# Performance work log

Hardware: AMD Instinct MI355X
Metric: run time of the kernel (lower is better)

The kernel has to match this reference:

```python
import jax, jax.numpy as jnp
import numpy as np

VOCAB, D, A, NEG = 32000, 200, 20, 2
NUM_USERS, NUM_ITEMS = 100000, 50000
R, L, B, NNZ = 4096, 128, 1024, 20480
EPS = 1e-12

def _norm(x, axis):
    n = jnp.sqrt(jnp.sum(x * x, axis=axis, keepdims=True))
    return x / jnp.maximum(n, EPS)

def setup_inputs() -> dict:
    key = jax.random.key(0)
    ks = jax.random.split(key, 20)
    rows_u = jax.random.randint(ks[5], (NNZ,), 0, B)
    cols_u = jax.random.randint(ks[6], (NNZ,), 0, R)
    rows_i = jax.random.randint(ks[7], (NNZ,), 0, B)
    cols_i = jax.random.randint(ks[8], (NNZ,), 0, R)
    return {
        "historical_review": jax.random.randint(ks[0], (R, L), 0, VOCAB),
        "neg_review": jax.random.randint(ks[1], (R * NEG, L), 0, VOCAB),
        "user": jax.random.randint(ks[2], (B,), 0, NUM_USERS),
        "item": jax.random.randint(ks[3], (B,), 0, NUM_ITEMS),
        "label": jax.random.uniform(ks[4], (B,), jnp.float32, 1.0, 5.0),
        "user_histor_index": jnp.stack([rows_u, cols_u]),
        "user_histor_value": jax.random.uniform(ks[9], (NNZ,), jnp.float32),
        "item_histor_index": jnp.stack([rows_i, cols_i]),
        "item_histor_value": jax.random.uniform(ks[10], (NNZ,), jnp.float32),
        "word_emb": jax.random.normal(ks[11], (VOCAB, D), jnp.float32),
        "Wm": jax.random.normal(ks[12], (D, D), jnp.float32) * 0.05,
        "Ww": jax.random.normal(ks[13], (A, D), jnp.float32) * 0.05,
        "bw": jnp.zeros((A,), jnp.float32),
        "Wt": jax.random.normal(ks[14], (D, A), jnp.float32) * 0.05,
        "fc_w": jax.random.uniform(ks[15], (1, 2 * D), jnp.float32, -0.05, 0.05),
        "fc_b": jnp.zeros((1,), jnp.float32),
        "fm_V": jax.random.uniform(ks[16], (2 * D, 10), jnp.float32, -0.05, 0.05),
        "b_users": jax.random.uniform(ks[17], (NUM_USERS, 1), jnp.float32, 0.0, 0.1),
        "b_items": jax.random.uniform(ks[18], (NUM_ITEMS, 1), jnp.float32, 0.0, 0.1),
    }

def reference(historical_review, neg_review, user, item, label,
              user_histor_index, user_histor_value,
              item_histor_index, item_histor_value,
              word_emb, Wm, Ww, bw, Wt, fc_w, fc_b, fm_V, b_users, b_items):
    # ABAE attention over each review
    e_w = word_emb[historical_review]              # (R, L, D)
    y_s = jnp.mean(e_w, axis=1)                    # (R, D)
    z_n = jnp.mean(word_emb[neg_review], axis=1)   # (R*NEG, D)
    dx = jnp.einsum('rld,rd->rl', e_w @ Wm.T, y_s) # (R, L)
    ax = jax.nn.softmax(dx, axis=1)
    # Faithful to source: view(R, D, L) is a raw reshape, not a transpose.
    z_s = jnp.einsum('rdl,rl->rd', e_w.reshape(R, D, L), ax)  # (R, D)
    p_t = z_s @ Ww.T + bw                          # (R, A)
    r_s = p_t @ Wt.T                               # (R, D)
    # cosine margin ranking loss
    c1 = jnp.sum(_norm(r_s, 1) * _norm(z_s, 1), axis=-1)      # (R,)
    c1 = jnp.repeat(c1, NEG)                                   # (R*NEG,)
    c2 = jnp.sum(_norm(z_n.reshape(R, NEG, D), 2) * _norm(r_s, 1)[:, None, :], axis=-1).reshape(-1)
    abae_out_loss = jax.nn.relu(c2 - c1 + 1.0)     # margin=1, target=+1
    J_loss = jnp.mean(abae_out_loss)
    # aspect-matrix orthogonality regularizer
    Tn = _norm(Wt, 0)                              # normalize columns (dim=0)
    U_loss = jnp.mean((Tn.T @ Tn - jnp.eye(A, dtype=Wt.dtype)) ** 2)
    # sparse (B, R) @ (R, D) aggregation via segment_sum
    user_aspect_embed = jax.ops.segment_sum(
        user_histor_value[:, None] * r_s[user_histor_index[1]],
        user_histor_index[0], num_segments=B)      # (B, D)
    item_aspect_embed = jax.ops.segment_sum(
        item_histor_value[:, None] * r_s[item_histor_index[1]],
        item_histor_index[0], num_segments=B)      # (B, D)
    input_vec = jnp.concatenate([user_aspect_embed, item_aspect_embed], axis=1)  # (B, 2D)
    fm_linear = input_vec @ fc_w.T + fc_b          # (B, 1)
    fm_i1 = (input_vec @ fm_V) ** 2
    fm_i2 = (input_vec ** 2) @ (fm_V ** 2)
    # NOTE: faithful to source, the quadratic term is summed over the whole batch (scalar)
    fm_output = 0.5 * jnp.sum(fm_i1 - fm_i2) + fm_linear + b_users[user] + b_items[item]
    prediction = fm_output.squeeze(1)              # (B,)
    rating_loss = (prediction - label) ** 2
    mse_loss = jnp.mean(rating_loss)
    obj_loss = mse_loss + 0.01 * J_loss + 0.01 * U_loss
    return (obj_loss, rating_loss, abae_out_loss, prediction, user_aspect_embed, item_aspect_embed)
```

## Files before the change

### kernel.cpp

```cpp
#include <hip/hip_runtime.h>
#include <hip/hip_fp16.h>
#include <math.h>

#define R_TOT 4096
#define L_LEN 128
#define D_DIM 200
#define A_DIM 20
#define NEGK  2
#define B_SZ  1024
#define NNZ_C 20480
#define RN_TOT (R_TOT*NEGK)
#define S_TOT (R_TOT + RN_TOT)
#define VOCAB_C 32000
#define EPS_ 1e-12f
#define SLOT_CAP 64
#define NBUCK_BLK 160

__device__ __forceinline__ float4 unpack4(const uint2 u) {
  union { unsigned v; __half2 h; } c0, c1;
  c0.v = u.x; c1.v = u.y;
  const float2 f0 = __half22float2(c0.h);
  const float2 f1 = __half22float2(c1.h);
  return make_float4(f0.x, f0.y, f1.x, f1.y);
}

__global__ __launch_bounds__(256) void k_cast(
    const float* __restrict__ emb, ushort* __restrict__ emb_h, int* __restrict__ cnt)
{
  if (blockIdx.x == 0) {
    for (int i = threadIdx.x; i < 2*B_SZ; i += 256) cnt[i] = 0;
  }
  const int idx = blockIdx.x*256 + threadIdx.x;
  if (idx < (VOCAB_C*D_DIM)/4) {
    const float4 v = reinterpret_cast<const float4*>(emb)[idx];
    ushort4 o;
    o.x = __half_as_ushort(__float2half(v.x));
    o.y = __half_as_ushort(__float2half(v.y));
    o.z = __half_as_ushort(__float2half(v.z));
    o.w = __half_as_ushort(__float2half(v.w));
    reinterpret_cast<ushort4*>(emb_h)[idx] = o;
  }
}

__global__ __launch_bounds__(256, 8) void k_means2(
    const int* __restrict__ hist, const int* __restrict__ neg,
    const ushort* __restrict__ emb_h,
    float* __restrict__ ys_all, float* __restrict__ zn_all,
    const int* __restrict__ uidx, const float* __restrict__ uval,
    const int* __restrict__ iidx, const float* __restrict__ ival,
    int* __restrict__ cnt, int* __restrict__ scol, float* __restrict__ sval)
{
  const int sb = blockIdx.x;
  const int tid = threadIdx.x;

  if (sb >= S_TOT) {
    const int g = (sb - S_TOT)*256 + tid;
    if (g < NNZ_C) {
      const int b = uidx[g];
      const int slot = atomicAdd(&cnt[b], 1);
      if (slot < SLOT_CAP) {
        scol[b*SLOT_CAP + slot] = uidx[NNZ_C + g];
        sval[b*SLOT_CAP + slot] = uval[g];
      }
    } else {
      const int g2 = g - NNZ_C;
      const int b = iidx[g2];
      const int slot = atomicAdd(&cnt[B_SZ + b], 1);
      if (slot < SLOT_CAP) {
        scol[(B_SZ + b)*SLOT_CAP + slot] = iidx[NNZ_C + g2];
        sval[(B_SZ + b)*SLOT_CAP + slot] = ival[g2];
      }
    }
    return;
  }

  __shared__ int widx[L_LEN];
  __shared__ __align__(16) float part[8][D_DIM];
  const bool is_pos = (sb < R_TOT);
  const int* src = is_pos ? (hist + (size_t)sb*L_LEN)
                          : (neg + (size_t)(sb - R_TOT)*L_LEN);
  if (tid < L_LEN) widx[tid] = src[tid];
  __syncthreads();

  const int c5 = tid & 31;
  const int j  = tid >> 5;
  float4 sA = {0.f,0.f,0.f,0.f}, sB = {0.f,0.f,0.f,0.f};
  if (c5 < 25) {
    const size_t coff = 8*c5;
    #pragma unroll
    for (int k0 = 0; k0 < 16; k0 += 4) {
      const uint4 q0 = *reinterpret_cast<const uint4*>(
          emb_h + (size_t)widx[j + 8*(k0+0)]*D_DIM + coff);
      const uint4 q1 = *reinterpret_cast<const uint4*>(
          emb_h + (size_t)widx[j + 8*(k0+1)]*D_DIM + coff);
      const uint4 q2 = *reinterpret_cast<const uint4*>(
          emb_h + (size_t)widx[j + 8*(k0+2)]*D_DIM + coff);
      const uint4 q3 = *reinterpret_cast<const uint4*>(
          emb_h + (size_t)widx[j + 8*(k0+3)]*D_DIM + coff);
      float4 e;
      e = unpack4(make_uint2(q0.x,q0.y)); sA.x+=e.x; sA.y+=e.y; sA.z+=e.z; sA.w+=e.w;
      e = unpack4(make_uint2(q0.z,q0.w)); sB.x+=e.x; sB.y+=e.y; sB.z+=e.z; sB.w+=e.w;
      e = unpack4(make_uint2(q1.x,q1.y)); sA.x+=e.x; sA.y+=e.y; sA.z+=e.z; sA.w+=e.w;
      e = unpack4(make_uint2(q1.z,q1.w)); sB.x+=e.x; sB.y+=e.y; sB.z+=e.z; sB.w+=e.w;
      e = unpack4(make_uint2(q2.x,q2.y)); sA.x+=e.x; sA.y+=e.y; sA.z+=e.z; sA.w+=e.w;
      e = unpack4(make_uint2(q2.z,q2.w)); sB.x+=e.x; sB.y+=e.y; sB.z+=e.z; sB.w+=e.w;
      e = unpack4(make_uint2(q3.x,q3.y)); sA.x+=e.x; sA.y+=e.y; sA.z+=e.z; sA.w+=e.w;
      e = unpack4(make_uint2(q3.z,q3.w)); sB.x+=e.x; sB.y+=e.y; sB.z+=e.z; sB.w+=e.w;
    }
    *reinterpret_cast<float4*>(&part[j][8*c5])     = sA;
    *reinterpret_cast<float4*>(&part[j][8*c5 + 4]) = sB;
  }
  __syncthreads();
  float* dst = is_pos ? (ys_all + (size_t)sb*D_DIM)
                      : (zn_all + (size_t)(sb - R_TOT)*D_DIM);
  if (tid < D_DIM) {
    float a = 0.f;
    #pragma unroll
    for (int j2 = 0; j2 < 8; ++j2) a += part[j2][tid];
    dst[tid] = a * (1.0f/128.0f);
  }
}

#define KB_RT 16
__global__ __launch_bounds__(256, 2) void k_matvec(
    const float* __restrict__ ys_all, const float* __restrict__ Wm,
    float* __restrict__ vv_all)
{
  __shared__ float ysl[KB_RT][D_DIM];
  const int r0 = blockIdx.x * KB_RT;
  const int tid = threadIdx.x;
  for (int i = tid; i < KB_RT*D_DIM; i += 256)
    ysl[i / D_DIM][i % D_DIM] = ys_all[(size_t)r0*D_DIM + i];
  __syncthreads();
  if (tid < D_DIM) {
    float acc[KB_RT];
    #pragma unroll
    for (int r = 0; r < KB_RT; ++r) acc[r] = 0.f;
    #pragma unroll 4
    for (int k = 0; k < D_DIM; ++k) {
      const float w = Wm[k*D_DIM + tid];
      #pragma unroll
      for (int r = 0; r < KB_RT; ++r) acc[r] += ysl[r][k] * w;
    }
    #pragma unroll
    for (int r = 0; r < KB_RT; ++r)
      vv_all[(size_t)(r0 + r)*D_DIM + tid] = acc[r];
  }
}

__global__ __launch_bounds__(512, 6) void k_attn(
    const int* __restrict__ hist, const ushort* __restrict__ emb_h,
    const float* __restrict__ vv_all,
    const float* __restrict__ Ww, const float* __restrict__ bw,
    const float* __restrict__ Wt, const float* __restrict__ zn_all,
    float* __restrict__ rs_out, float* __restrict__ abae)
{
  __shared__ __align__(16) ushort ew[L_LEN*D_DIM];
  __shared__ __align__(16) float ax[L_LEN];
  __shared__ __align__(16) float zs[D_DIM];
  __shared__ __align__(16) float ubuf[240];
  int*   widx  = reinterpret_cast<int*>(ubuf);
  float* ptile = ubuf;
  float* red   = ubuf + 160;

  const int r = blockIdx.x;
  const int tid = threadIdx.x, lane = tid & 63, wv = tid >> 6;

  if (tid < L_LEN) widx[tid] = hist[r*L_LEN + tid];
  __syncthreads();

  {
    const int c5 = tid & 31;
    const int j  = tid >> 5;
    float4 v8a = {0,0,0,0}, v8b = {0,0,0,0};
    if (c5 < 25) {
      v8a = *reinterpret_cast<const float4*>(vv_all + (size_t)r*D_DIM + 8*c5);
      v8b = *reinterpret_cast<const float4*>(vv_all + (size_t)r*D_DIM + 8*c5 + 4);
    }
    float p0=0.f,p1=0.f,p2=0.f,p3=0.f,p4=0.f,p5=0.f,p6=0.f,p7=0.f;
    if (c5 < 25) {
      const size_t coff = 8*c5;
      #pragma unroll
      for (int k = 0; k < 8; ++k) {
        const int l = j + 16*k;
        const uint4 q = *reinterpret_cast<const uint4*>(
            emb_h + (size_t)widx[l]*D_DIM + coff);
        *reinterpret_cast<uint4*>(ew + l*D_DIM + coff) = q;
        const float4 e0 = unpack4(make_uint2(q.x, q.y));
        const float4 e1 = unpack4(make_uint2(q.z, q.w));
        const float d = e0.x*v8a.x + e0.y*v8a.y + e0.z*v8a.z + e0.w*v8a.w
                      + e1.x*v8b.x + e1.y*v8b.y + e1.z*v8b.z + e1.w*v8b.w;
        if (k==0) p0=d; else if (k==1) p1=d; else if (k==2) p2=d; else if (k==3) p3=d;
        else if (k==4) p4=d; else if (k==5) p5=d; else if (k==6) p6=d; else p7=d;
      }
    }
    #pragma unroll
    for (int o = 16; o > 0; o >>= 1) {
      p0 += __shfl_xor(p0, o); p1 += __shfl_xor(p1, o);
      p2 += __shfl_xor(p2, o); p3 += __shfl_xor(p3, o);
      p4 += __shfl_xor(p4, o); p5 += __shfl_xor(p5, o);
      p6 += __shfl_xor(p6, o); p7 += __shfl_xor(p7, o);
    }
    if (c5 == 0) {
      ax[j]      = p0; ax[j + 16]  = p1; ax[j + 32]  = p2; ax[j + 48]  = p3;
      ax[j + 64] = p4; ax[j + 80]  = p5; ax[j + 96]  = p6; ax[j + 112] = p7;
    }
  }
  __syncthreads();

  if (tid < 64) {
    float m = fmaxf(ax[tid], ax[tid+64]);
    #pragma unroll
    for (int o = 32; o > 0; o >>= 1) m = fmaxf(m, __shfl_xor(m, o));
    if (tid == 0) red[0] = m;
  }
  __syncthreads();
  const float M = red[0];
  if (tid < L_LEN) ax[tid] = expf(ax[tid] - M);
  __syncthreads();
  if (tid < 64) {
    float s = ax[tid] + ax[tid+64];
    #pragma unroll
    for (int o = 32; o > 0; o >>= 1) s += __shfl_xor(s, o);
    if (tid == 0) red[1] = s;
  }
  __syncthreads();
  const float Sinv = 1.0f / red[1];
  if (tid < L_LEN) ax[tid] *= Sinv;
  __syncthreads();

  {
    const int lq = lane & 15;
    const int quad = lane >> 4;
    const float4 ax8a = *reinterpret_cast<const float4*>(ax + 8*lq);
    const float4 ax8b = *reinterpret_cast<const float4*>(ax + 8*lq + 4);
    for (int dq = wv; dq < 50; dq += 8) {
      const int d0 = 4*dq + quad;
      const int f0 = (d0 << 7) + 8*lq;
      const uint4 q = *reinterpret_cast<const uint4*>(ew + f0);
      const float4 e0 = unpack4(make_uint2(q.x, q.y));
      const float4 e1 = unpack4(make_uint2(q.z, q.w));
      float a = e0.x*ax8a.x + e0.y*ax8a.y + e0.z*ax8a.z + e0.w*ax8a.w
              + e1.x*ax8b.x + e1.y*ax8b.y + e1.z*ax8b.z + e1.w*ax8b.w;
      #pragma unroll
      for (int o = 8; o > 0; o >>= 1) a += __shfl_xor(a, o);
      if (lq == 0) zs[d0] = a;
    }
  }
  __syncthreads();

  if (tid < 160) {
    const int a = tid % 20, j = tid / 20;
    float s = 0.f;
    #pragma unroll
    for (int i = 0; i < 25; ++i) {
      const int d = j + 8*i;
      s += zs[d] * Ww[a*D_DIM + d];
    }
    ptile[tid] = s;
  }
  __syncthreads();
  if (tid < A_DIM) {
    float s = bw[tid];
    #pragma unroll
    for (int j = 0; j < 8; ++j) s += ptile[j*20 + tid];
    red[2 + tid] = s;
  }
  __syncthreads();

  float rsd = 0.f, zsd = 0.f, zn0 = 0.f, zn1 = 0.f;
  if (tid < D_DIM) {
    float acc = 0.f;
    #pragma unroll
    for (int a = 0; a < A_DIM; ++a) acc += red[2+a] * Wt[tid*A_DIM + a];
    rsd = acc; zsd = zs[tid];
    rs_out[(size_t)r*D_DIM + tid] = acc;
    zn0 = zn_all[(size_t)(2*r)*D_DIM + tid];
    zn1 = zn_all[(size_t)(2*r + 1)*D_DIM + tid];
  }
  float a0 = rsd*rsd, a1 = zsd*zsd, a2 = rsd*zsd;
  float b0 = zn0*zn0, b1 = zn0*rsd, b2 = zn1*zn1, b3 = zn1*rsd;
  #pragma unroll
  for (int o = 32; o > 0; o >>= 1) {
    a0 += __shfl_xor(a0, o); a1 += __shfl_xor(a1, o); a2 += __shfl_xor(a2, o);
    b0 += __shfl_xor(b0, o); b1 += __shfl_xor(b1, o);
    b2 += __shfl_xor(b2, o); b3 += __shfl_xor(b3, o);
  }
  if ((tid & 63) == 0) {
    red[22+wv] = a0; red[30+wv] = a1; red[38+wv] = a2;
    red[46+wv] = b0; red[54+wv] = b1; red[62+wv] = b2; red[70+wv] = b3;
  }
  __syncthreads();
  if (tid == 0) {
    float s0=0.f,s1=0.f,s2=0.f,t0=0.f,t1=0.f,t2=0.f,t3=0.f;
    #pragma unroll
    for (int i = 0; i < 8; ++i) {
      s0 += red[22+i]; s1 += red[30+i]; s2 += red[38+i];
      t0 += red[46+i]; t1 += red[54+i]; t2 += red[62+i]; t3 += red[70+i];
    }
    const float nr = fmaxf(sqrtf(s0), EPS_);
    const float nz = fmaxf(sqrtf(s1), EPS_);
    const float c1 = s2 / (nr * nz);
    const float c2a = t1 / (fmaxf(sqrtf(t0), EPS_) * nr);
    const float c2b = t3 / (fmaxf(sqrtf(t2), EPS_) * nr);
    abae[2*r]     = fmaxf(c2a - c1 + 1.0f, 0.0f);
    abae[2*r + 1] = fmaxf(c2b - c1 + 1.0f, 0.0f);
  }
}

__global__ __launch_bounds__(512) void k_aggfm(
    const int* __restrict__ cnt, const int* __restrict__ scol,
    const float* __restrict__ sval, const float* __restrict__ rs,
    const float* __restrict__ fcw, const float* __restrict__ V,
    float* __restrict__ uae, float* __restrict__ iae,
    float* __restrict__ linb, float* __restrict__ quadb)
{
  __shared__ __align__(16) float ivec[2*D_DIM];
  __shared__ float redw[8];
  __shared__ float qpart[10];
  const int b = blockIdx.x;
  const int tid = threadIdx.x, lane = tid & 63, wv = tid >> 6;

  if (tid < D_DIM) {
    int n = cnt[b]; n = n < SLOT_CAP ? n : SLOT_CAP;
    const int* cols = scol + (size_t)b*SLOT_CAP;
    const float* vals = sval + (size_t)b*SLOT_CAP;
    float acc = 0.f;
    for (int j = 0; j < n; ++j) acc += vals[j] * rs[(size_t)cols[j]*D_DIM + tid];
    ivec[tid] = acc;
    uae[(size_t)b*D_DIM + tid] = acc;
  } else if (tid >= 256 && tid < 256 + D_DIM) {
    const int t = tid - 256;
    int n = cnt[B_SZ + b]; n = n < SLOT_CAP ? n : SLOT_CAP;
    const int* cols = scol + (size_t)(B_SZ + b)*SLOT_CAP;
    const float* vals = sval + (size_t)(B_SZ + b)*SLOT_CAP;
    float acc = 0.f;
    for (int j = 0; j < n; ++j) acc += vals[j] * rs[(size_t)cols[j]*D_DIM + t];
    ivec[D_DIM + t] = acc;
    iae[(size_t)b*D_DIM + t] = acc;
  }
  __syncthreads();

  float lv = 0.f;
  if (tid < 2*D_DIM) lv = ivec[tid] * fcw[tid];
  #pragma unroll
  for (int o = 32; o > 0; o >>= 1) lv += __shfl_xor(lv, o);
  if (lane == 0) redw[wv] = lv;

  {
    const int k = wv;
    float s1 = 0.f, s2 = 0.f;
    for (int f = lane; f < 2*D_DIM; f += 64) {
      const float x = ivec[f];
      const float vk = V[f*10 + k];
      s1 += x*vk; s2 += x*x*vk*vk;
    }
    #pragma unroll
    for (int o = 32; o > 0; o >>= 1) { s1 += __shfl_xor(s1,o); s2 += __shfl_xor(s2,o); }
    if (lane == 0) qpart[k] = s1*s1 - s2;
  }
  if (wv < 2) {
    const int k = 8 + wv;
    float s1 = 0.f, s2 = 0.f;
    for (int f = lane; f < 2*D_DIM; f += 64) {
      const float x = ivec[f];
      const float vk = V[f*10 + k];
      s1 += x*vk; s2 += x*x*vk*vk;
    }
    #pragma unroll
    for (int o = 32; o > 0; o >>= 1) { s1 += __shfl_xor(s1,o); s2 += __shfl_xor(s2,o); }
    if (lane == 0) qpart[k] = s1*s1 - s2;
  }
  __syncthreads();
  if (tid == 0) {
    float lin = 0.f;
    #pragma unroll
    for (int i = 0; i < 8; ++i) lin += redw[i];
    float q = 0.f;
    #pragma unroll
    for (int i = 0; i < 10; ++i) q += qpart[i];
    linb[b] = lin; quadb[b] = q;
  }
}

__global__ __launch_bounds__(1024) void k_final2(
    const float* __restrict__ quadb, const float* __restrict__ linb,
    const float* __restrict__ fcb, const int* __restrict__ user,
    const int* __restrict__ item, const float* __restrict__ busers,
    const float* __restrict__ bitems, const float* __restrict__ label,
    const float* __restrict__ Wt, const float* __restrict__ abae,
    float* __restrict__ pred, float* __restrict__ rl, float* __restrict__ obj)
{
  __shared__ float sA[16], sB[16], sC[16];
  __shared__ float cninv[A_DIM];
  __shared__ float quad_s;
  const int tid = threadIdx.x;
  const int lane = tid & 63;
  const int wv = tid >> 6;

  float q = quadb[tid];
  #pragma unroll
  for (int o = 32; o > 0; o >>= 1) q += __shfl_xor(q, o);
  if (lane == 0) sA[wv] = q;

  if (tid < A_DIM) {
    float s = 0.f;
    for (int d = 0; d < D_DIM; ++d) { const float w = Wt[d*A_DIM + tid]; s += w*w; }
    cninv[tid] = 1.0f / fmaxf(sqrtf(s), EPS_);
  }
  __syncthreads();
  if (wv == 0) {
    float s = (lane < 16) ? sA[lane] : 0.f;
    #pragma unroll
    for (int o = 32; o > 0; o >>= 1) s += __shfl_xor(s, o);
    if (lane == 0) quad_s = s;
  }
  __syncthreads();

  const float p = 0.5f*quad_s + linb[tid] + fcb[0]
                + busers[user[tid]] + bitems[item[tid]];
  pred[tid] = p;
  const float dd = p - label[tid];
  const float myrl = dd*dd;
  rl[tid] = myrl;

  float u = 0.f;
  if (tid < 400) {
    const int a = tid / 20, c = tid % 20;
    float dot = 0.f;
    for (int d = 0; d < D_DIM; ++d) dot += Wt[d*A_DIM + a]*Wt[d*A_DIM + c];
    const float g = dot*cninv[a]*cninv[c] - (a==c ? 1.0f : 0.0f);
    u = g*g;
  }
  float js = 0.f;
  #pragma unroll
  for (int j = 0; j < 8; ++j) js += abae[tid + 1024*j];
  float ms = myrl;

  #pragma unroll
  for (int o = 32; o > 0; o >>= 1) {
    u += __shfl_xor(u,o); js += __shfl_xor(js,o); ms += __shfl_xor(ms,o);
  }
  if (lane == 0) { sA[wv] = u; sB[wv] = js; sC[wv] = ms; }
  __syncthreads();
  if (tid == 0) {
    float U = 0.f, J = 0.f, Ms = 0.f;
    for (int i = 0; i < 16; ++i) { U += sA[i]; J += sB[i]; Ms += sC[i]; }
    obj[0] = Ms/1024.0f + 0.01f*(J/8192.0f) + 0.01f*(U/400.0f);
  }
}

extern "C" void kernel_launch(void* const* d_in, const int* in_sizes, int n_in,
                              void* d_out, int out_size, void* d_ws, size_t ws_size,
                              hipStream_t stream) {
  const int*   hist   = (const int*)  d_in[0];
  const int*   neg    = (const int*)  d_in[1];
  const int*   user   = (const int*)  d_in[2];
  const int*   item   = (const int*)  d_in[3];
  const float* label  = (const float*)d_in[4];
  const int*   uidx   = (const int*)  d_in[5];
  const float* uval   = (const float*)d_in[6];
  const int*   iidx   = (const int*)  d_in[7];
  const float* ival   = (const float*)d_in[8];
  const float* emb    = (const float*)d_in[9];
  const float* Wm     = (const float*)d_in[10];
  const float* Ww     = (const float*)d_in[11];
  const float* bw     = (const float*)d_in[12];
  const float* Wt     = (const float*)d_in[13];
  const float* fcw    = (const float*)d_in[14];
  const float* fcb    = (const float*)d_in[15];
  const float* V      = (const float*)d_in[16];
  const float* busers = (const float*)d_in[17];
  const float* bitems = (const float*)d_in[18];

  float* out  = (float*)d_out;
  float* obj  = out;
  float* rl   = out + 1;
  float* abae = out + 1 + B_SZ;
  float* pred = out + 1 + B_SZ + RN_TOT;
  float* uae  = pred + B_SZ;
  float* iae  = uae + (size_t)B_SZ*D_DIM;

  float* ws     = (float*)d_ws;
  float* rs     = ws;
  float* ys_all = rs + (size_t)R_TOT*D_DIM;
  float* zn_all = ys_all + (size_t)R_TOT*D_DIM;
  float* vv_all = zn_all + (size_t)RN_TOT*D_DIM;
  float* linb   = vv_all + (size_t)R_TOT*D_DIM;
  float* quadb  = linb + B_SZ;
  float* sval   = quadb + B_SZ;
  int*   scol   = (int*)(sval + (size_t)2*B_SZ*SLOT_CAP);
  int*   cnt    = scol + (size_t)2*B_SZ*SLOT_CAP;
  ushort* emb_h = (ushort*)(cnt + 2*B_SZ);

  const int cast_blocks = (VOCAB_C*D_DIM/4 + 255)/256;

  k_cast  <<<cast_blocks, 256, 0, stream>>>(emb, emb_h, cnt);
  k_means2<<<S_TOT + NBUCK_BLK, 256, 0, stream>>>(hist, neg, emb_h,
                                                  ys_all, zn_all,
                                                  uidx, uval, iidx, ival,
                                                  cnt, scol, sval);
  k_matvec<<<R_TOT/KB_RT, 256, 0, stream>>>(ys_all, Wm, vv_all);
  k_attn  <<<R_TOT, 512, 0, stream>>>(hist, emb_h, vv_all, Ww, bw, Wt,
                                      zn_all, rs, abae);
  k_aggfm <<<B_SZ, 512, 0, stream>>>(cnt, scol, sval, rs, fcw, V,
                                     uae, iae, linb, quadb);
  k_final2<<<1, 1024, 0, stream>>>(quadb, linb, fcb, user, item, busers, bitems,
                                   label, Wt, abae, pred, rl, obj);
}
```

Before: 312.5 us.

## Process four reviews per attention block with register prefetch of next embeddings

The attention kernel now handles four reviews per block in a loop. While it computes the current review, it prefetches the next review's word indices, fp16 embedding rows, vv vector and zn values into registers. The goal is to hide gather latency behind the softmax and reduction stages and to cut block launch and index-staging overhead. In exchange the grid has a quarter as many blocks, register pressure rises from holding eight uint4 prefetches, and occupancy and parallelism across the GPU's compute units may drop.

```diff
diff --git a/kernel.cpp b/kernel.cpp
--- a/kernel.cpp
+++ b/kernel.cpp
@@ -15,6 +15,7 @@
 #define EPS_ 1e-12f
 #define SLOT_CAP 64
 #define NBUCK_BLK 160
+#define NREV 4
 
 __device__ __forceinline__ float4 unpack4(const uint2 u) {
   union { unsigned v; __half2 h; } c0, c1;
@@ -159,41 +160,80 @@
   __shared__ __align__(16) float ax[L_LEN];
   __shared__ __align__(16) float zs[D_DIM];
   __shared__ __align__(16) float ubuf[240];
-  int*   widx  = reinterpret_cast<int*>(ubuf);
   float* ptile = ubuf;
   float* red   = ubuf + 160;
 
-  const int r = blockIdx.x;
   const int tid = threadIdx.x, lane = tid & 63, wv = tid >> 6;
-
-  if (tid < L_LEN) widx[tid] = hist[r*L_LEN + tid];
-  __syncthreads();
-
-  {
-    const int c5 = tid & 31;
-    const int j  = tid >> 5;
-    float4 v8a = {0,0,0,0}, v8b = {0,0,0,0};
-    if (c5 < 25) {
-      v8a = *reinterpret_cast<const float4*>(vv_all + (size_t)r*D_DIM + 8*c5);
-      v8b = *reinterpret_cast<const float4*>(vv_all + (size_t)r*D_DIM + 8*c5 + 4);
-    }
+  const int c5 = tid & 31;
+  const int j  = tid >> 5;
+  const bool act = (c5 < 25);
+  const int coff = 8*c5;
+  const int r0 = blockIdx.x * NREV;
+
+  uint4 q0,q1,q2,q3,q4,q5,q6,q7;
+  q0=q1=q2=q3=q4=q5=q6=q7=make_uint4(0,0,0,0);
+  float4 v8a = {0,0,0,0}, v8b = {0,0,0,0};
+  if (act) {
+    const int base = r0*L_LEN + j;
+    const int w0 = hist[base],     w1 = hist[base+16], w2 = hist[base+32], w3 = hist[base+48];
+    const int w4 = hist[base+64],  w5 = hist[base+80], w6 = hist[base+96], w7 = hist[base+112];
+    q0 = *reinterpret_cast<const uint4*>(emb_h + (size_t)w0*D_DIM + coff);
+    q1 = *reinterpret_cast<const uint4*>(emb_h + (size_t)w1*D_DIM + coff);
+    q2 = *reinterpret_cast<const uint4*>(emb_h + (size_t)w2*D_DIM + coff);
+    q3 = *reinterpret_cast<const uint4*>(emb_h + (size_t)w3*D_DIM + coff);
+    q4 = *reinterpret_cast<const uint4*>(emb_h + (size_t)w4*D_DIM + coff);
+    q5 = *reinterpret_cast<const uint4*>(emb_h + (size_t)w5*D_DIM + coff);
+    q6 = *reinterpret_cast<const uint4*>(emb_h + (size_t)w6*D_DIM + coff);
+    q7 = *reinterpret_cast<const uint4*>(emb_h + (size_t)w7*D_DIM + coff);
+    v8a = *reinterpret_cast<const float4*>(vv_all + (size_t)r0*D_DIM + coff);
+    v8b = *reinterpret_cast<const float4*>(vv_all + (size_t)r0*D_DIM + coff + 4);
+  }
+
+  for (int i = 0; i < NREV; ++i) {
+    const int r = r0 + i;
+
+    int w0n=0,w1n=0,w2n=0,w3n=0,w4n=0,w5n=0,w6n=0,w7n=0;
+    if (act && i < NREV-1) {
+      const int nb = (r+1)*L_LEN + j;
+      w0n = hist[nb];     w1n = hist[nb+16]; w2n = hist[nb+32]; w3n = hist[nb+48];
+      w4n = hist[nb+64];  w5n = hist[nb+80]; w6n = hist[nb+96]; w7n = hist[nb+112];
+    }
+
+    __syncthreads();
+
     float p0=0.f,p1=0.f,p2=0.f,p3=0.f,p4=0.f,p5=0.f,p6=0.f,p7=0.f;
-    if (c5 < 25) {
-      const size_t coff = 8*c5;
-      #pragma unroll
-      for (int k = 0; k < 8; ++k) {
-        const int l = j + 16*k;
-        const uint4 q = *reinterpret_cast<const uint4*>(
-            emb_h + (size_t)widx[l]*D_DIM + coff);
-        *reinterpret_cast<uint4*>(ew + l*D_DIM + coff) = q;
-        const float4 e0 = unpack4(make_uint2(q.x, q.y));
-        const float4 e1 = unpack4(make_uint2(q.z, q.w));
-        const float d = e0.x*v8a.x + e0.y*v8a.y + e0.z*v8a.z + e0.w*v8a.w
-                      + e1.x*v8b.x + e1.y*v8b.y + e1.z*v8b.z + e1.w*v8b.w;
-        if (k==0) p0=d; else if (k==1) p1=d; else if (k==2) p2=d; else if (k==3) p3=d;
-        else if (k==4) p4=d; else if (k==5) p5=d; else if (k==6) p6=d; else p7=d;
+    if (act) {
+      #define STG(K, Q, P) { \
+        *reinterpret_cast<uint4*>(ew + (j + 16*(K))*D_DIM + coff) = Q; \
+        const float4 e0_ = unpack4(make_uint2(Q.x, Q.y)); \
+        const float4 e1_ = unpack4(make_uint2(Q.z, Q.w)); \
+        P = e0_.x*v8a.x + e0_.y*v8a.y + e0_.z*v8a.z + e0_.w*v8a.w \
+          + e1_.x*v8b.x + e1_.y*v8b.y + e1_.z*v8b.z + e1_.w*v8b.w; }
+      STG(0,q0,p0) STG(1,q1,p1) STG(2,q2,p2) STG(3,q3,p3)
+      STG(4,q4,p4) STG(5,q5,p5) STG(6,q6,p6) STG(7,q7,p7)
+      #undef STG
+      if (i < NREV-1) {
+        q0 = *reinterpret_cast<const uint4*>(emb_h + (size_t)w0n*D_DIM + coff);
+        q1 = *reinterpret_cast<const uint4*>(emb_h + (size_t)w1n*D_DIM + coff);
+        q2 = *reinterpret_cast<const uint4*>(emb_h + (size_t)w2n*D_DIM + coff);
+        q3 = *reinterpret_cast<const uint4*>(emb_h + (size_t)w3n*D_DIM + coff);
+        q4 = *reinterpret_cast<const uint4*>(emb_h + (size_t)w4n*D_DIM + coff);
+        q5 = *reinterpret_cast<const uint4*>(emb_h + (size_t)w5n*D_DIM + coff);
+        q6 = *reinterpret_cast<const uint4*>(emb_h + (size_t)w6n*D_DIM + coff);
+        q7 = *reinterpret_cast<const uint4*>(emb_h + (size_t)w7n*D_DIM + coff);
       }
     }
+    float4 v8an = {0,0,0,0}, v8bn = {0,0,0,0};
+    if (act && i < NREV-1) {
+      v8an = *reinterpret_cast<const float4*>(vv_all + (size_t)(r+1)*D_DIM + coff);
+      v8bn = *reinterpret_cast<const float4*>(vv_all + (size_t)(r+1)*D_DIM + coff + 4);
+    }
+    float zn0 = 0.f, zn1 = 0.f;
+    if (tid < D_DIM) {
+      zn0 = zn_all[(size_t)(2*r)*D_DIM + tid];
+      zn1 = zn_all[(size_t)(2*r + 1)*D_DIM + tid];
+    }
+
     #pragma unroll
     for (int o = 16; o > 0; o >>= 1) {
       p0 += __shfl_xor(p0, o); p1 += __shfl_xor(p1, o);
@@ -205,106 +245,106 @@
       ax[j]      = p0; ax[j + 16]  = p1; ax[j + 32]  = p2; ax[j + 48]  = p3;
       ax[j + 64] = p4; ax[j + 80]  = p5; ax[j + 96]  = p6; ax[j + 112] = p7;
     }
-  }
-  __syncthreads();
-
-  if (tid < 64) {
-    float m = fmaxf(ax[tid], ax[tid+64]);
-    #pragma unroll
-    for (int o = 32; o > 0; o >>= 1) m = fmaxf(m, __shfl_xor(m, o));
-    if (tid == 0) red[0] = m;
-  }
-  __syncthreads();
-  const float M = red[0];
-  if (tid < L_LEN) ax[tid] = expf(ax[tid] - M);
-  __syncthreads();
-  if (tid < 64) {
-    float s = ax[tid] + ax[tid+64];
-    #pragma unroll
-    for (int o = 32; o > 0; o >>= 1) s += __shfl_xor(s, o);
-    if (tid == 0) red[1] = s;
-  }
-  __syncthreads();
-  const float Sinv = 1.0f / red[1];
-  if (tid < L_LEN) ax[tid] *= Sinv;
-  __syncthreads();
-
-  {
-    const int lq = lane & 15;
-    const int quad = lane >> 4;
-    const float4 ax8a = *reinterpret_cast<const float4*>(ax + 8*lq);
-    const float4 ax8b = *reinterpret_cast<const float4*>(ax + 8*lq + 4);
-    for (int dq = wv; dq < 50; dq += 8) {
-      const int d0 = 4*dq + quad;
-      const int f0 = (d0 << 7) + 8*lq;
-      const uint4 q = *reinterpret_cast<const uint4*>(ew + f0);
-      const float4 e0 = unpack4(make_uint2(q.x, q.y));
-      const float4 e1 = unpack4(make_uint2(q.z, q.w));
-      float a = e0.x*ax8a.x + e0.y*ax8a.y + e0.z*ax8a.z + e0.w*ax8a.w
-              + e1.x*ax8b.x + e1.y*ax8b.y + e1.z*ax8b.z + e1.w*ax8b.w;
-      #pragma unroll
-      for (int o = 8; o > 0; o >>= 1) a += __shfl_xor(a, o);
-      if (lq == 0) zs[d0] = a;
-    }
-  }
-  __syncthreads();
-
-  if (tid < 160) {
-    const int a = tid % 20, j = tid / 20;
-    float s = 0.f;
-    #pragma unroll
-    for (int i = 0; i < 25; ++i) {
-      const int d = j + 8*i;
-      s += zs[d] * Ww[a*D_DIM + d];
-    }
-    ptile[tid] = s;
-  }
-  __syncthreads();
-  if (tid < A_DIM) {
-    float s = bw[tid];
-    #pragma unroll
-    for (int j = 0; j < 8; ++j) s += ptile[j*20 + tid];
-    red[2 + tid] = s;
-  }
-  __syncthreads();
-
-  float rsd = 0.f, zsd = 0.f, zn0 = 0.f, zn1 = 0.f;
-  if (tid < D_DIM) {
-    float acc = 0.f;
-    #pragma unroll
-    for (int a = 0; a < A_DIM; ++a) acc += red[2+a] * Wt[tid*A_DIM + a];
-    rsd = acc; zsd = zs[tid];
-    rs_out[(size_t)r*D_DIM + tid] = acc;
-    zn0 = zn_all[(size_t)(2*r)*D_DIM + tid];
-    zn1 = zn_all[(size_t)(2*r + 1)*D_DIM + tid];
-  }
-  float a0 = rsd*rsd, a1 = zsd*zsd, a2 = rsd*zsd;
-  float b0 = zn0*zn0, b1 = zn0*rsd, b2 = zn1*zn1, b3 = zn1*rsd;
-  #pragma unroll
-  for (int o = 32; o > 0; o >>= 1) {
-    a0 += __shfl_xor(a0, o); a1 += __shfl_xor(a1, o); a2 += __shfl_xor(a2, o);
-    b0 += __shfl_xor(b0, o); b1 += __shfl_xor(b1, o);
-    b2 += __shfl_xor(b2, o); b3 += __shfl_xor(b3, o);
-  }
-  if ((tid & 63) == 0) {
-    red[22+wv] = a0; red[30+wv] = a1; red[38+wv] = a2;
-    red[46+wv] = b0; red[54+wv] = b1; red[62+wv] = b2; red[70+wv] = b3;
-  }
-  __syncthreads();
-  if (tid == 0) {
-    float s0=0.f,s1=0.f,s2=0.f,t0=0.f,t1=0.f,t2=0.f,t3=0.f;
-    #pragma unroll
-    for (int i = 0; i < 8; ++i) {
-      s0 += red[22+i]; s1 += red[30+i]; s2 += red[38+i];
-      t0 += red[46+i]; t1 += red[54+i]; t2 += red[62+i]; t3 += red[70+i];
-    }
-    const float nr = fmaxf(sqrtf(s0), EPS_);
-    const float nz = fmaxf(sqrtf(s1), EPS_);
-    const float c1 = s2 / (nr * nz);
-    const float c2a = t1 / (fmaxf(sqrtf(t0), EPS_) * nr);
-    const float c2b = t3 / (fmaxf(sqrtf(t2), EPS_) * nr);
-    abae[2*r]     = fmaxf(c2a - c1 + 1.0f, 0.0f);
-    abae[2*r + 1] = fmaxf(c2b - c1 + 1.0f, 0.0f);
+    __syncthreads();
+
+    if (tid < 64) {
+      float m = fmaxf(ax[tid], ax[tid+64]);
+      #pragma unroll
+      for (int o = 32; o > 0; o >>= 1) m = fmaxf(m, __shfl_xor(m, o));
+      if (tid == 0) red[0] = m;
+    }
+    __syncthreads();
+    const float M = red[0];
+    if (tid < L_LEN) ax[tid] = expf(ax[tid] - M);
+    __syncthreads();
+    if (tid < 64) {
+      float s = ax[tid] + ax[tid+64];
+      #pragma unroll
+      for (int o = 32; o > 0; o >>= 1) s += __shfl_xor(s, o);
+      if (tid == 0) red[1] = s;
+    }
+    __syncthreads();
+    const float Sinv = 1.0f / red[1];
+    if (tid < L_LEN) ax[tid] *= Sinv;
+    __syncthreads();
+
+    {
+      const int lq = lane & 15;
+      const int quad = lane >> 4;
+      const float4 ax8a = *reinterpret_cast<const float4*>(ax + 8*lq);
+      const float4 ax8b = *reinterpret_cast<const float4*>(ax + 8*lq + 4);
+      for (int dq = wv; dq < 50; dq += 8) {
+        const int d0 = 4*dq + quad;
+        const int f0 = (d0 << 7) + 8*lq;
+        const uint4 q = *reinterpret_cast<const uint4*>(ew + f0);
+        const float4 e0 = unpack4(make_uint2(q.x, q.y));
+        const float4 e1 = unpack4(make_uint2(q.z, q.w));
+        float a = e0.x*ax8a.x + e0.y*ax8a.y + e0.z*ax8a.z + e0.w*ax8a.w
+                + e1.x*ax8b.x + e1.y*ax8b.y + e1.z*ax8b.z + e1.w*ax8b.w;
+        #pragma unroll
+        for (int o = 8; o > 0; o >>= 1) a += __shfl_xor(a, o);
+        if (lq == 0) zs[d0] = a;
+      }
+    }
+    __syncthreads();
+
+    if (tid < 160) {
+      const int a = tid % 20, jj = tid / 20;
+      float s = 0.f;
+      #pragma unroll
+      for (int ii = 0; ii < 25; ++ii) {
+        const int d = jj + 8*ii;
+        s += zs[d] * Ww[a*D_DIM + d];
+      }
+      ptile[tid] = s;
+    }
+    __syncthreads();
+    if (tid < A_DIM) {
+      float s = bw[tid];
+      #pragma unroll
+      for (int jj = 0; jj < 8; ++jj) s += ptile[jj*20 + tid];
+      red[2 + tid] = s;
+    }
+    __syncthreads();
+
+    float rsd = 0.f, zsd = 0.f;
+    if (tid < D_DIM) {
+      float acc = 0.f;
+      #pragma unroll
+      for (int a = 0; a < A_DIM; ++a) acc += red[2+a] * Wt[tid*A_DIM + a];
+      rsd = acc; zsd = zs[tid];
+      rs_out[(size_t)r*D_DIM + tid] = acc;
+    } else { zn0 = 0.f; zn1 = 0.f; }
+    float a0 = rsd*rsd, a1 = zsd*zsd, a2 = rsd*zsd;
+    float b0 = zn0*zn0, b1 = zn0*rsd, b2 = zn1*zn1, b3 = zn1*rsd;
+    #pragma unroll
+    for (int o = 32; o > 0; o >>= 1) {
+      a0 += __shfl_xor(a0, o); a1 += __shfl_xor(a1, o); a2 += __shfl_xor(a2, o);
+      b0 += __shfl_xor(b0, o); b1 += __shfl_xor(b1, o);
+      b2 += __shfl_xor(b2, o); b3 += __shfl_xor(b3, o);
+    }
+    if ((tid & 63) == 0) {
+      red[22+wv] = a0; red[30+wv] = a1; red[38+wv] = a2;
+      red[46+wv] = b0; red[54+wv] = b1; red[62+wv] = b2; red[70+wv] = b3;
+    }
+    __syncthreads();
+    if (tid == 0) {
+      float s0=0.f,s1=0.f,s2=0.f,t0=0.f,t1=0.f,t2=0.f,t3=0.f;
+      #pragma unroll
+      for (int ii = 0; ii < 8; ++ii) {
+        s0 += red[22+ii]; s1 += red[30+ii]; s2 += red[38+ii];
+        t0 += red[46+ii]; t1 += red[54+ii]; t2 += red[62+ii]; t3 += red[70+ii];
+      }
+      const float nr = fmaxf(sqrtf(s0), EPS_);
+      const float nz = fmaxf(sqrtf(s1), EPS_);
+      const float c1 = s2 / (nr * nz);
+      const float c2a = t1 / (fmaxf(sqrtf(t0), EPS_) * nr);
+      const float c2b = t3 / (fmaxf(sqrtf(t2), EPS_) * nr);
+      abae[2*r]     = fmaxf(c2a - c1 + 1.0f, 0.0f);
+      abae[2*r + 1] = fmaxf(c2b - c1 + 1.0f, 0.0f);
+    }
+
+    v8a = v8an; v8b = v8bn;
   }
 }
 
@@ -501,8 +541,8 @@
                                                   uidx, uval, iidx, ival,
                                                   cnt, scol, sval);
   k_matvec<<<R_TOT/KB_RT, 256, 0, stream>>>(ys_all, Wm, vv_all);
-  k_attn  <<<R_TOT, 512, 0, stream>>>(hist, emb_h, vv_all, Ww, bw, Wt,
-                                      zn_all, rs, abae);
+  k_attn  <<<R_TOT/NREV, 512, 0, stream>>>(hist, emb_h, vv_all, Ww, bw, Wt,
+                                           zn_all, rs, abae);
   k_aggfm <<<B_SZ, 512, 0, stream>>>(cnt, scol, sval, rs, fcw, V,
                                      uae, iae, linb, quadb);
   k_final2<<<1, 1024, 0, stream>>>(quadb, linb, fcb, user, item, busers, bitems,
```

After: 630.5 us. 2.02x slower.

## Batch gather loads and trim softmax barriers in means and attention kernels

Applied to the files above, without the earlier changes.

The mean kernel now issues eight independent embedding-row loads before accumulating, replacing the previous batches of four, to raise memory-level parallelism. The attention kernel hoists the vv and zn loads ahead of the first barrier and issues all eight row gathers up front. It fuses the softmax exp and sum into one pass, folding normalization into the zs write so two barriers disappear. The final reduction now uses shuffles instead of a serial loop on one thread. Occupancy hint for k_attn drops from 6 to 4 waves per SIMD to allow more registers. The cost is higher register pressure and possibly fewer resident blocks.

```diff
diff --git a/kernel.cpp b/kernel.cpp
--- a/kernel.cpp
+++ b/kernel.cpp
@@ -41,6 +41,12 @@
     reinterpret_cast<ushort4*>(emb_h)[idx] = o;
   }
 }
+
+#define ACC8(Q) { \
+  const float4 e0_ = unpack4(make_uint2((Q).x,(Q).y)); \
+  const float4 e1_ = unpack4(make_uint2((Q).z,(Q).w)); \
+  sA.x+=e0_.x; sA.y+=e0_.y; sA.z+=e0_.z; sA.w+=e0_.w; \
+  sB.x+=e1_.x; sB.y+=e1_.y; sB.z+=e1_.z; sB.w+=e1_.w; }
 
 __global__ __launch_bounds__(256, 8) void k_means2(
     const int* __restrict__ hist, const int* __restrict__ neg,
@@ -87,26 +93,24 @@
   float4 sA = {0.f,0.f,0.f,0.f}, sB = {0.f,0.f,0.f,0.f};
   if (c5 < 25) {
     const size_t coff = 8*c5;
-    #pragma unroll
-    for (int k0 = 0; k0 < 16; k0 += 4) {
-      const uint4 q0 = *reinterpret_cast<const uint4*>(
-          emb_h + (size_t)widx[j + 8*(k0+0)]*D_DIM + coff);
-      const uint4 q1 = *reinterpret_cast<const uint4*>(
-          emb_h + (size_t)widx[j + 8*(k0+1)]*D_DIM + coff);
-      const uint4 q2 = *reinterpret_cast<const uint4*>(
-          emb_h + (size_t)widx[j + 8*(k0+2)]*D_DIM + coff);
-      const uint4 q3 = *reinterpret_cast<const uint4*>(
-          emb_h + (size_t)widx[j + 8*(k0+3)]*D_DIM + coff);
-      float4 e;
-      e = unpack4(make_uint2(q0.x,q0.y)); sA.x+=e.x; sA.y+=e.y; sA.z+=e.z; sA.w+=e.w;
-      e = unpack4(make_uint2(q0.z,q0.w)); sB.x+=e.x; sB.y+=e.y; sB.z+=e.z; sB.w+=e.w;
-      e = unpack4(make_uint2(q1.x,q1.y)); sA.x+=e.x; sA.y+=e.y; sA.z+=e.z; sA.w+=e.w;
-      e = unpack4(make_uint2(q1.z,q1.w)); sB.x+=e.x; sB.y+=e.y; sB.z+=e.z; sB.w+=e.w;
-      e = unpack4(make_uint2(q2.x,q2.y)); sA.x+=e.x; sA.y+=e.y; sA.z+=e.z; sA.w+=e.w;
-      e = unpack4(make_uint2(q2.z,q2.w)); sB.x+=e.x; sB.y+=e.y; sB.z+=e.z; sB.w+=e.w;
-      e = unpack4(make_uint2(q3.x,q3.y)); sA.x+=e.x; sA.y+=e.y; sA.z+=e.z; sA.w+=e.w;
-      e = unpack4(make_uint2(q3.z,q3.w)); sB.x+=e.x; sB.y+=e.y; sB.z+=e.z; sB.w+=e.w;
-    }
+    uint4 q0 = *reinterpret_cast<const uint4*>(emb_h + (size_t)widx[j +   0]*D_DIM + coff);
+    uint4 q1 = *reinterpret_cast<const uint4*>(emb_h + (size_t)widx[j +   8]*D_DIM + coff);
+    uint4 q2 = *reinterpret_cast<const uint4*>(emb_h + (size_t)widx[j +  16]*D_DIM + coff);
+    uint4 q3 = *reinterpret_cast<const uint4*>(emb_h + (size_t)widx[j +  24]*D_DIM + coff);
+    uint4 q4 = *reinterpret_cast<const uint4*>(emb_h + (size_t)widx[j +  32]*D_DIM + coff);
+    uint4 q5 = *reinterpret_cast<const uint4*>(emb_h + (size_t)widx[j +  40]*D_DIM + coff);
+    uint4 q6 = *reinterpret_cast<const uint4*>(emb_h + (size_t)widx[j +  48]*D_DIM + coff);
+    uint4 q7 = *reinterpret_cast<const uint4*>(emb_h + (size_t)widx[j +  56]*D_DIM + coff);
+    ACC8(q0) ACC8(q1) ACC8(q2) ACC8(q3) ACC8(q4) ACC8(q5) ACC8(q6) ACC8(q7)
+    q0 = *reinterpret_cast<const uint4*>(emb_h + (size_t)widx[j +  64]*D_DIM + coff);
+    q1 = *reinterpret_cast<const uint4*>(emb_h + (size_t)widx[j +  72]*D_DIM + coff);
+    q2 = *reinterpret_cast<const uint4*>(emb_h + (size_t)widx[j +  80]*D_DIM + coff);
+    q3 = *reinterpret_cast<const uint4*>(emb_h + (size_t)widx[j +  88]*D_DIM + coff);
+    q4 = *reinterpret_cast<const uint4*>(emb_h + (size_t)widx[j +  96]*D_DIM + coff);
+    q5 = *reinterpret_cast<const uint4*>(emb_h + (size_t)widx[j + 104]*D_DIM + coff);
+    q6 = *reinterpret_cast<const uint4*>(emb_h + (size_t)widx[j + 112]*D_DIM + coff);
+    q7 = *reinterpret_cast<const uint4*>(emb_h + (size_t)widx[j + 120]*D_DIM + coff);
+    ACC8(q0) ACC8(q1) ACC8(q2) ACC8(q3) ACC8(q4) ACC8(q5) ACC8(q6) ACC8(q7)
     *reinterpret_cast<float4*>(&part[j][8*c5])     = sA;
     *reinterpret_cast<float4*>(&part[j][8*c5 + 4]) = sB;
   }
@@ -148,7 +152,7 @@
   }
 }
 
-__global__ __launch_bounds__(512, 6) void k_attn(
+__global__ __launch_bounds__(512, 4) void k_attn(
     const int* __restrict__ hist, const ushort* __restrict__ emb_h,
     const float* __restrict__ vv_all,
     const float* __restrict__ Ww, const float* __restrict__ bw,
@@ -165,46 +169,59 @@
 
   const int r = blockIdx.x;
   const int tid = threadIdx.x, lane = tid & 63, wv = tid >> 6;
+  const int c5 = tid & 31;
+  const int j  = tid >> 5;
+  const bool act = (c5 < 25);
+  const int coff = 8*c5;
 
   if (tid < L_LEN) widx[tid] = hist[r*L_LEN + tid];
-  __syncthreads();
-
+  float4 v8a = {0,0,0,0}, v8b = {0,0,0,0};
+  if (act) {
+    v8a = *reinterpret_cast<const float4*>(vv_all + (size_t)r*D_DIM + coff);
+    v8b = *reinterpret_cast<const float4*>(vv_all + (size_t)r*D_DIM + coff + 4);
+  }
+  __syncthreads();
+
+  float zn0 = 0.f, zn1 = 0.f;
+  float p0=0.f,p1=0.f,p2=0.f,p3=0.f,p4=0.f,p5=0.f,p6=0.f,p7=0.f;
   {
-    const int c5 = tid & 31;
-    const int j  = tid >> 5;
-    float4 v8a = {0,0,0,0}, v8b = {0,0,0,0};
-    if (c5 < 25) {
-      v8a = *reinterpret_cast<const float4*>(vv_all + (size_t)r*D_DIM + 8*c5);
-      v8b = *reinterpret_cast<const float4*>(vv_all + (size_t)r*D_DIM + 8*c5 + 4);
-    }
-    float p0=0.f,p1=0.f,p2=0.f,p3=0.f,p4=0.f,p5=0.f,p6=0.f,p7=0.f;
-    if (c5 < 25) {
-      const size_t coff = 8*c5;
-      #pragma unroll
-      for (int k = 0; k < 8; ++k) {
-        const int l = j + 16*k;
-        const uint4 q = *reinterpret_cast<const uint4*>(
-            emb_h + (size_t)widx[l]*D_DIM + coff);
-        *reinterpret_cast<uint4*>(ew + l*D_DIM + coff) = q;
-        const float4 e0 = unpack4(make_uint2(q.x, q.y));
-        const float4 e1 = unpack4(make_uint2(q.z, q.w));
-        const float d = e0.x*v8a.x + e0.y*v8a.y + e0.z*v8a.z + e0.w*v8a.w
-                      + e1.x*v8b.x + e1.y*v8b.y + e1.z*v8b.z + e1.w*v8b.w;
-        if (k==0) p0=d; else if (k==1) p1=d; else if (k==2) p2=d; else if (k==3) p3=d;
-        else if (k==4) p4=d; else if (k==5) p5=d; else if (k==6) p6=d; else p7=d;
-      }
-    }
-    #pragma unroll
-    for (int o = 16; o > 0; o >>= 1) {
-      p0 += __shfl_xor(p0, o); p1 += __shfl_xor(p1, o);
-      p2 += __shfl_xor(p2, o); p3 += __shfl_xor(p3, o);
-      p4 += __shfl_xor(p4, o); p5 += __shfl_xor(p5, o);
-      p6 += __shfl_xor(p6, o); p7 += __shfl_xor(p7, o);
-    }
-    if (c5 == 0) {
-      ax[j]      = p0; ax[j + 16]  = p1; ax[j + 32]  = p2; ax[j + 48]  = p3;
-      ax[j + 64] = p4; ax[j + 80]  = p5; ax[j + 96]  = p6; ax[j + 112] = p7;
-    }
+    uint4 q0,q1,q2,q3,q4,q5,q6,q7;
+    if (act) {
+      q0 = *reinterpret_cast<const uint4*>(emb_h + (size_t)widx[j +   0]*D_DIM + coff);
+      q1 = *reinterpret_cast<const uint4*>(emb_h + (size_t)widx[j +  16]*D_DIM + coff);
+      q2 = *reinterpret_cast<const uint4*>(emb_h + (size_t)widx[j +  32]*D_DIM + coff);
+      q3 = *reinterpret_cast<const uint4*>(emb_h + (size_t)widx[j +  48]*D_DIM + coff);
+      q4 = *reinterpret_cast<const uint4*>(emb_h + (size_t)widx[j +  64]*D_DIM + coff);
+      q5 = *reinterpret_cast<const uint4*>(emb_h + (size_t)widx[j +  80]*D_DIM + coff);
+      q6 = *reinterpret_cast<const uint4*>(emb_h + (size_t)widx[j +  96]*D_DIM + coff);
+      q7 = *reinterpret_cast<const uint4*>(emb_h + (size_t)widx[j + 112]*D_DIM + coff);
+    }
+    if (tid < D_DIM) {
+      zn0 = zn_all[(size_t)(2*r)*D_DIM + tid];
+      zn1 = zn_all[(size_t)(2*r + 1)*D_DIM + tid];
+    }
+    if (act) {
+      #define STG(K, Q, P) { \
+        *reinterpret_cast<uint4*>(ew + (j + 16*(K))*D_DIM + coff) = Q; \
+        const float4 e0_ = unpack4(make_uint2(Q.x, Q.y)); \
+        const float4 e1_ = unpack4(make_uint2(Q.z, Q.w)); \
+        P = e0_.x*v8a.x + e0_.y*v8a.y + e0_.z*v8a.z + e0_.w*v8a.w \
+          + e1_.x*v8b.x + e1_.y*v8b.y + e1_.z*v8b.z + e1_.w*v8b.w; }
+      STG(0,q0,p0) STG(1,q1,p1) STG(2,q2,p2) STG(3,q3,p3)
+      STG(4,q4,p4) STG(5,q5,p5) STG(6,q6,p6) STG(7,q7,p7)
+      #undef STG
+    }
+  }
+  #pragma unroll
+  for (int o = 16; o > 0; o >>= 1) {
+    p0 += __shfl_xor(p0, o); p1 += __shfl_xor(p1, o);
+    p2 += __shfl_xor(p2, o); p3 += __shfl_xor(p3, o);
+    p4 += __shfl_xor(p4, o); p5 += __shfl_xor(p5, o);
+    p6 += __shfl_xor(p6, o); p7 += __shfl_xor(p7, o);
+  }
+  if (c5 == 0) {
+    ax[j]      = p0; ax[j + 16]  = p1; ax[j + 32]  = p2; ax[j + 48]  = p3;
+    ax[j + 64] = p4; ax[j + 80]  = p5; ax[j + 96]  = p6; ax[j + 112] = p7;
   }
   __syncthreads();
 
@@ -216,20 +233,18 @@
   }
   __syncthreads();
   const float M = red[0];
-  if (tid < L_LEN) ax[tid] = expf(ax[tid] - M);
-  __syncthreads();
-  if (tid < 64) {
-    float s = ax[tid] + ax[tid+64];
+  if (tid < L_LEN) {
+    float e = expf(ax[tid] - M);
+    ax[tid] = e;
+    float s = e;
     #pragma unroll
     for (int o = 32; o > 0; o >>= 1) s += __shfl_xor(s, o);
-    if (tid == 0) red[1] = s;
-  }
-  __syncthreads();
-  const float Sinv = 1.0f / red[1];
-  if (tid < L_LEN) ax[tid] *= Sinv;
+    if (lane == 0) red[1 + wv] = s;
+  }
   __syncthreads();
 
   {
+    const float Sinv = 1.0f / (red[1] + red[2]);
     const int lq = lane & 15;
     const int quad = lane >> 4;
     const float4 ax8a = *reinterpret_cast<const float4*>(ax + 8*lq);
@@ -244,17 +259,17 @@
               + e1.x*ax8b.x + e1.y*ax8b.y + e1.z*ax8b.z + e1.w*ax8b.w;
       #pragma unroll
       for (int o = 8; o > 0; o >>= 1) a += __shfl_xor(a, o);
-      if (lq == 0) zs[d0] = a;
+      if (lq == 0) zs[d0] = a * Sinv;
     }
   }
   __syncthreads();
 
   if (tid < 160) {
-    const int a = tid % 20, j = tid / 20;
+    const int a = tid % 20, jj = tid / 20;
     float s = 0.f;
     #pragma unroll
-    for (int i = 0; i < 25; ++i) {
-      const int d = j + 8*i;
+    for (int ii = 0; ii < 25; ++ii) {
+      const int d = jj + 8*ii;
       s += zs[d] * Ww[a*D_DIM + d];
     }
     ptile[tid] = s;
@@ -263,21 +278,19 @@
   if (tid < A_DIM) {
     float s = bw[tid];
     #pragma unroll
-    for (int j = 0; j < 8; ++j) s += ptile[j*20 + tid];
+    for (int jj = 0; jj < 8; ++jj) s += ptile[jj*20 + tid];
     red[2 + tid] = s;
   }
   __syncthreads();
 
-  float rsd = 0.f, zsd = 0.f, zn0 = 0.f, zn1 = 0.f;
+  float rsd = 0.f, zsd = 0.f;
   if (tid < D_DIM) {
     float acc = 0.f;
     #pragma unroll
     for (int a = 0; a < A_DIM; ++a) acc += red[2+a] * Wt[tid*A_DIM + a];
     rsd = acc; zsd = zs[tid];
     rs_out[(size_t)r*D_DIM + tid] = acc;
-    zn0 = zn_all[(size_t)(2*r)*D_DIM + tid];
-    zn1 = zn_all[(size_t)(2*r + 1)*D_DIM + tid];
-  }
+  } else { zn0 = 0.f; zn1 = 0.f; }
   float a0 = rsd*rsd, a1 = zsd*zsd, a2 = rsd*zsd;
   float b0 = zn0*zn0, b1 = zn0*rsd, b2 = zn1*zn1, b3 = zn1*rsd;
   #pragma unroll
@@ -286,25 +299,29 @@
     b0 += __shfl_xor(b0, o); b1 += __shfl_xor(b1, o);
     b2 += __shfl_xor(b2, o); b3 += __shfl_xor(b3, o);
   }
-  if ((tid & 63) == 0) {
-    red[22+wv] = a0; red[30+wv] = a1; red[38+wv] = a2;
-    red[46+wv] = b0; red[54+wv] = b1; red[62+wv] = b2; red[70+wv] = b3;
-  }
-  __syncthreads();
-  if (tid == 0) {
-    float s0=0.f,s1=0.f,s2=0.f,t0=0.f,t1=0.f,t2=0.f,t3=0.f;
-    #pragma unroll
-    for (int i = 0; i < 8; ++i) {
-      s0 += red[22+i]; s1 += red[30+i]; s2 += red[38+i];
-      t0 += red[46+i]; t1 += red[54+i]; t2 += red[62+i]; t3 += red[70+i];
-    }
-    const float nr = fmaxf(sqrtf(s0), EPS_);
-    const float nz = fmaxf(sqrtf(s1), EPS_);
-    const float c1 = s2 / (nr * nz);
-    const float c2a = t1 / (fmaxf(sqrtf(t0), EPS_) * nr);
-    const float c2b = t3 / (fmaxf(sqrtf(t2), EPS_) * nr);
-    abae[2*r]     = fmaxf(c2a - c1 + 1.0f, 0.0f);
-    abae[2*r + 1] = fmaxf(c2b - c1 + 1.0f, 0.0f);
+  if (lane == 0) {
+    red[22 + 0*8 + wv] = a0; red[22 + 1*8 + wv] = a1; red[22 + 2*8 + wv] = a2;
+    red[22 + 3*8 + wv] = b0; red[22 + 4*8 + wv] = b1;
+    red[22 + 5*8 + wv] = b2; red[22 + 6*8 + wv] = b3;
+  }
+  __syncthreads();
+
+  if (tid < 64) {
+    const int qi = tid >> 3, k = tid & 7;
+    float v = (qi < 7) ? red[22 + 8*qi + k] : 0.f;
+    v += __shfl_xor(v, 1); v += __shfl_xor(v, 2); v += __shfl_xor(v, 4);
+    const float s0 = __shfl(v, 0),  s1 = __shfl(v, 8),  s2 = __shfl(v, 16);
+    const float t0 = __shfl(v, 24), t1 = __shfl(v, 32);
+    const float t2 = __shfl(v, 40), t3 = __shfl(v, 48);
+    if (tid == 0) {
+      const float nr = fmaxf(sqrtf(s0), EPS_);
+      const float nz = fmaxf(sqrtf(s1), EPS_);
+      const float c1 = s2 / (nr * nz);
+      const float c2a = t1 / (fmaxf(sqrtf(t0), EPS_) * nr);
+      const float c2b = t3 / (fmaxf(sqrtf(t2), EPS_) * nr);
+      abae[2*r]     = fmaxf(c2a - c1 + 1.0f, 0.0f);
+      abae[2*r + 1] = fmaxf(c2b - c1 + 1.0f, 0.0f);
+    }
   }
 }
 
```

New measurement: 309.2 us. Within noise of the previous version (-1.0%).
